# Kernel tuning notes

Measured on AMD Instinct MI355X. Metric: run time of the kernel, lower is better.

The kernel has to match this reference:

```python
import jax, jax.numpy as jnp
import numpy as np

EMB, HEADS, K, GADD, RADD = 256, 8, 8, 2, 2
REGION, STRIDE = 64, 32
MIN_SIGMA, SIGMA_SCALE, SIGMA_BOOST = 0.05, 0.1, 2.0
MMULT = 1.0 * 3.0  # clamp=True triples mmult in __init__
B, T = 4, 4096


def setup_inputs() -> dict:
    key = jax.random.key(0)
    ks = jax.random.split(key, 8)
    def lin(k, fi, fo):
        return jax.random.normal(k, (fi, fo), jnp.float32) / np.sqrt(fi).astype(np.float32)
    return {
        "x": jax.random.normal(ks[0], (B, T, EMB), jnp.float32),
        "Wq": lin(ks[1], EMB, EMB * HEADS),
        "Wk": lin(ks[2], EMB, EMB * HEADS),
        "Wv": lin(ks[3], EMB, EMB * HEADS),
        "Wu": lin(ks[4], EMB * HEADS, EMB),
        "bu": jnp.zeros((EMB,), jnp.float32),
        "W1": lin(ks[5], EMB + 1, 4 * EMB),
        "b1": jnp.zeros((4 * EMB,), jnp.float32),
        "W2": lin(ks[6], 4 * EMB, 2 * K) * 0.1,
        "b2": jnp.zeros((2 * K,), jnp.float32),
    }


def _forward(x, Wq, Wk, Wv, Wu, bu, W1, b1, W2, b2):
    b, t, e = x.shape
    h, k, r = HEADS, K, STRIDE
    tp = t // r
    vs = k * (2 + GADD + RADD)
    sel = (jnp.arange(tp) + 1) * r - 1  # query positions (tp,)

    # --- hyper network: k Gaussian means/sigmas per (strided) query position ---
    coords = jnp.broadcast_to((jnp.arange(tp, dtype=jnp.float32) / tp)[None, :, None], (b, tp, 1))
    inp = jnp.concatenate([x[:, sel, :], coords], axis=2)            # (b,tp,e+1)
    params = jax.nn.relu(inp @ W1 + b1) @ W2 + b2                    # (b,tp,2k)
    diags = sel.astype(jnp.float32)[None, :, None]                   # (1,tp,1)
    means = diags - MMULT * jax.nn.softplus(params[:, :, :k])        # (b,tp,k), left of diagonal
    means = jnp.clip(means, 0.0, t - 1.0)                            # transform_means 'clamp'
    sigmas = (jax.nn.softplus(params[:, :, k:] + SIGMA_BOOST) + MIN_SIGMA) * t * SIGMA_SCALE

    # --- ngenerate: 2 integer neighbours + global + regional samples per Gaussian ---
    kg, kr = jax.random.split(jax.random.key(42))
    fl = jnp.floor(means)                                            # (b,tp,k)
    neigh = jnp.stack([fl, fl + 1.0], axis=-1)                       # (b,tp,k,2)
    gidx = jax.random.randint(kg, (b, tp, k, GADD), 0, t).astype(jnp.float32)
    lo = jnp.clip(fl - REGION // 2, 0.0, float(t - REGION))
    ridx = lo[..., None] + jax.random.randint(kr, (b, tp, k, RADD), 0, REGION).astype(jnp.float32)
    idxf = jnp.concatenate([neigh, gidx, ridx], axis=-1)             # (b,tp,k,2+G+R)
    indices = jnp.clip(idxf, 0, t - 1).astype(jnp.int32).reshape(b, tp, vs)

    # --- densities of every sampled index under every mixture component ---
    indfl = indices.astype(jnp.float32)
    z = (indfl[:, :, :, None] - means[:, :, None, :]) / sigmas[:, :, None, :]
    props = jnp.exp(-0.5 * z * z)                                    # (b,tp,vs,k)

    # zero duplicates (keep first occurrence) and acausal indices
    eq = indices[:, :, :, None] == indices[:, :, None, :]            # (b,tp,vs,vs)
    tri = np.tril(np.ones((vs, vs), dtype=bool), -1)
    dup = jnp.any(eq & tri[None, None], axis=-1)                     # (b,tp,vs)
    valid = (~dup) & (indices <= sel[None, :, None])
    props = jnp.where(valid[..., None], props, 0.0)
    props = props / props.sum(axis=2, keepdims=True)
    weights = props.sum(axis=3)                                      # mvalues == 1 -> (b,tp,vs)

    # --- per-head projections (each head has full emb dim) ---
    scale = e ** 0.25
    qh = (x @ Wq).reshape(b, t, h, e).transpose(0, 2, 1, 3) / scale  # (b,h,t,e)
    kh = (x @ Wk).reshape(b, t, h, e).transpose(0, 2, 1, 3) / scale
    vh = (x @ Wv).reshape(b, t, h, e).transpose(0, 2, 1, 3)

    # gather sparse key/value rows
    ki = jnp.broadcast_to(indices.reshape(b, 1, tp * vs, 1), (b, h, tp * vs, e))
    skeys = jnp.take_along_axis(kh, ki, axis=2).reshape(b, h, tp, vs, e)
    svals = jnp.take_along_axis(vh, ki, axis=2).reshape(b, h, tp, vs, e)
    qsel = qh[:, :, sel, :]                                          # (b,h,tp,e)

    dot = jnp.einsum('bhpe,bhpve->bhpv', qsel, skeys)                # sparse dot products
    att = jax.nn.softmax(weights[:, None] * dot, axis=-1)            # sparse row logsoftmax().exp()
    outp = jnp.einsum('bhpv,bhpve->bhpe', att, svals)                # sparse batchmm

    out = jnp.zeros((b, h, t, e), x.dtype).at[:, :, sel, :].set(outp)
    out = out.transpose(0, 2, 1, 3).reshape(b, t, h * e)
    return out @ Wu + bu


def reference(x, Wq, Wk, Wv, Wu, bu, W1, b1, W2, b2):
    return _forward(x, Wq, Wk, Wv, Wu, bu, W1, b1, W2, b2)
```

## Files before the change

kernel.cpp:

```cpp
#include <hip/hip_runtime.h>
#include <stdint.h>

#define EMB   256
#define HEADS 8
#define KMIX  8
#define GADD  2
#define RADD  2
#define REGION 64
#define STRIDE 32
#define BB    4
#define TT    4096
#define TP    128
#define VS    48
#define HID   1024
#define NQ    2048

__device__ __forceinline__ uint32_t rotl32(uint32_t x, int d) {
  return (x << d) | (x >> (32 - d));
}
__device__ __forceinline__ void tf2x32(uint32_t k0, uint32_t k1,
                                       uint32_t x0, uint32_t x1,
                                       uint32_t& o0, uint32_t& o1) {
  uint32_t ks2 = k0 ^ k1 ^ 0x1BD11BDAu;
  x0 += k0; x1 += k1;
#define TFR(r) { x0 += x1; x1 = rotl32(x1, r); x1 ^= x0; }
  TFR(13) TFR(15) TFR(26) TFR(6)
  x0 += k1; x1 += ks2 + 1u;
  TFR(17) TFR(29) TFR(16) TFR(24)
  x0 += ks2; x1 += k0 + 2u;
  TFR(13) TFR(15) TFR(26) TFR(6)
  x0 += k0; x1 += k1 + 3u;
  TFR(17) TFR(29) TFR(16) TFR(24)
  x0 += k1; x1 += ks2 + 4u;
  TFR(13) TFR(15) TFR(26) TFR(6)
  x0 += ks2; x1 += k0 + 5u;
#undef TFR
  o0 = x0; o1 = x1;
}

__device__ __forceinline__ size_t selrow(int m) {
  return (size_t)(m >> 7) * TT + ((m & 127) * STRIDE + STRIDE - 1);
}

__global__ __launch_bounds__(256) void phase1_kernel(
    const float* __restrict__ Wq, const float* __restrict__ Wk,
    const float* __restrict__ Wv, const float* __restrict__ Wu,
    const float* __restrict__ x,  const float* __restrict__ W1,
    float* __restrict__ M8, float* __restrict__ PV, float* __restrict__ hid0)
{
  const int bid = blockIdx.x;
  const int tid = threadIdx.x;
  const int tx = tid & 15, ty = tid >> 4;

  __shared__ float As[32][33];
  __shared__ __align__(16) float Braw[64 * 33];

  float acc[2][4];
#pragma unroll
  for (int i = 0; i < 2; i++)
#pragma unroll
    for (int j = 0; j < 4; j++) acc[i][j] = 0.0f;

  if (bid < 512) {
    const int zz = bid >> 5, rem = bid & 31;
    const int n0 = (rem & 3) * 64, m0 = (rem >> 2) * 32;
    if (zz < HEADS) {
      const float* A = Wq + zz * 256;
      const float* B = Wk + zz * 256;
      float* C = M8 + (size_t)zz * EMB * EMB;
      for (int k0 = 0; k0 < EMB; k0 += 32) {
        {
          int r = tid >> 3, kq = tid & 7;
          float4 v = *(const float4*)(A + (size_t)(m0 + r) * NQ + k0 + kq * 4);
          As[r][kq * 4 + 0] = v.x; As[r][kq * 4 + 1] = v.y;
          As[r][kq * 4 + 2] = v.z; As[r][kq * 4 + 3] = v.w;
        }
#pragma unroll
        for (int rr = 0; rr < 2; rr++) {
          int c = tid * 2 + rr;
          int r = c >> 3, kq = c & 7;
          float4 v = *(const float4*)(B + (size_t)(n0 + r) * NQ + k0 + kq * 4);
          Braw[r * 33 + kq * 4 + 0] = v.x; Braw[r * 33 + kq * 4 + 1] = v.y;
          Braw[r * 33 + kq * 4 + 2] = v.z; Braw[r * 33 + kq * 4 + 3] = v.w;
        }
        __syncthreads();
#pragma unroll
        for (int kk = 0; kk < 32; kk++) {
          float a0 = As[ty * 2 + 0][kk], a1 = As[ty * 2 + 1][kk];
          float b0 = Braw[(tx * 4 + 0) * 33 + kk];
          float b1 = Braw[(tx * 4 + 1) * 33 + kk];
          float b2 = Braw[(tx * 4 + 2) * 33 + kk];
          float b3 = Braw[(tx * 4 + 3) * 33 + kk];
          acc[0][0] = fmaf(a0, b0, acc[0][0]); acc[0][1] = fmaf(a0, b1, acc[0][1]);
          acc[0][2] = fmaf(a0, b2, acc[0][2]); acc[0][3] = fmaf(a0, b3, acc[0][3]);
          acc[1][0] = fmaf(a1, b0, acc[1][0]); acc[1][1] = fmaf(a1, b1, acc[1][1]);
          acc[1][2] = fmaf(a1, b2, acc[1][2]); acc[1][3] = fmaf(a1, b3, acc[1][3]);
        }
        __syncthreads();
      }
#pragma unroll
      for (int i = 0; i < 2; i++) {
        float* cp = C + (size_t)(m0 + ty * 2 + i) * EMB + n0 + tx * 4;
        *(float4*)cp = make_float4(acc[i][0] * 0.0625f, acc[i][1] * 0.0625f,
                                   acc[i][2] * 0.0625f, acc[i][3] * 0.0625f);
      }
    } else {
      const int hh = zz - HEADS;
      const float* A = Wv + hh * 256;
      const float* W = Wu + (size_t)hh * 256 * EMB;
      float* C = PV + (size_t)hh * EMB * EMB;
      for (int k0 = 0; k0 < EMB; k0 += 32) {
        {
          int r = tid >> 3, kq = tid & 7;
          float4 v = *(const float4*)(A + (size_t)(m0 + r) * NQ + k0 + kq * 4);
          As[r][kq * 4 + 0] = v.x; As[r][kq * 4 + 1] = v.y;
          As[r][kq * 4 + 2] = v.z; As[r][kq * 4 + 3] = v.w;
        }
#pragma unroll
        for (int rr = 0; rr < 2; rr++) {
          int c = tid * 2 + rr;
          int kk = c >> 4, n4 = c & 15;
          *(float4*)(&Braw[kk * 64 + n4 * 4]) =
              *(const float4*)(W + (size_t)(k0 + kk) * EMB + n0 + n4 * 4);
        }
        __syncthreads();
#pragma unroll
        for (int kk = 0; kk < 32; kk++) {
          float a0 = As[ty * 2 + 0][kk], a1 = As[ty * 2 + 1][kk];
          float4 b4 = *(const float4*)&Braw[kk * 64 + tx * 4];
          acc[0][0] = fmaf(a0, b4.x, acc[0][0]); acc[0][1] = fmaf(a0, b4.y, acc[0][1]);
          acc[0][2] = fmaf(a0, b4.z, acc[0][2]); acc[0][3] = fmaf(a0, b4.w, acc[0][3]);
          acc[1][0] = fmaf(a1, b4.x, acc[1][0]); acc[1][1] = fmaf(a1, b4.y, acc[1][1]);
          acc[1][2] = fmaf(a1, b4.z, acc[1][2]); acc[1][3] = fmaf(a1, b4.w, acc[1][3]);
        }
        __syncthreads();
      }
#pragma unroll
      for (int i = 0; i < 2; i++) {
        float* cp = C + (size_t)(m0 + ty * 2 + i) * EMB + n0 + tx * 4;
        *(float4*)cp = make_float4(acc[i][0], acc[i][1], acc[i][2], acc[i][3]);
      }
    }
  } else {
    const int idx = bid - 512;
    const int n0 = (idx & 15) * 64, m0 = (idx >> 4) * 32;
    for (int k0 = 0; k0 < EMB; k0 += 32) {
      {
        int r = tid >> 3, kq = tid & 7;
        float4 v = *(const float4*)(x + selrow(m0 + r) * EMB + k0 + kq * 4);
        As[r][kq * 4 + 0] = v.x; As[r][kq * 4 + 1] = v.y;
        As[r][kq * 4 + 2] = v.z; As[r][kq * 4 + 3] = v.w;
      }
#pragma unroll
      for (int rr = 0; rr < 2; rr++) {
        int c = tid * 2 + rr;
        int kk = c >> 4, n4 = c & 15;
        *(float4*)(&Braw[kk * 64 + n4 * 4]) =
            *(const float4*)(W1 + (size_t)(k0 + kk) * HID + n0 + n4 * 4);
      }
      __syncthreads();
#pragma unroll
      for (int kk = 0; kk < 32; kk++) {
        float a0 = As[ty * 2 + 0][kk], a1 = As[ty * 2 + 1][kk];
        float4 b4 = *(const float4*)&Braw[kk * 64 + tx * 4];
        acc[0][0] = fmaf(a0, b4.x, acc[0][0]); acc[0][1] = fmaf(a0, b4.y, acc[0][1]);
        acc[0][2] = fmaf(a0, b4.z, acc[0][2]); acc[0][3] = fmaf(a0, b4.w, acc[0][3]);
        acc[1][0] = fmaf(a1, b4.x, acc[1][0]); acc[1][1] = fmaf(a1, b4.y, acc[1][1]);
        acc[1][2] = fmaf(a1, b4.z, acc[1][2]); acc[1][3] = fmaf(a1, b4.w, acc[1][3]);
      }
      __syncthreads();
    }
#pragma unroll
    for (int i = 0; i < 2; i++) {
      float* cp = hid0 + (size_t)(m0 + ty * 2 + i) * HID + n0 + tx * 4;
      *(float4*)cp = make_float4(acc[i][0], acc[i][1], acc[i][2], acc[i][3]);
    }
  }
}

__device__ __forceinline__ float softplus_f(float v) {
  return fmaxf(v, 0.0f) + log1pf(expf(-fabsf(v)));
}

__global__ __launch_bounds__(256) void phase2_kernel(
    const float* __restrict__ x,  const float* __restrict__ M8,
    const float* __restrict__ hid0,
    const float* __restrict__ W1, const float* __restrict__ b1,
    const float* __restrict__ W2, const float* __restrict__ b2,
    float* __restrict__ qk, int* __restrict__ idx_out, float* __restrict__ w_out)
{
  const int bid = blockIdx.x;
  const int tid = threadIdx.x;

  if (bid < 512) {
    const int h = bid >> 6, rem = bid & 63;
    const int n0 = (rem & 3) * 64, m0 = (rem >> 2) * 32;
    const int tx = tid & 15, ty = tid >> 4;
    const float* W = M8 + (size_t)h * EMB * EMB;

    __shared__ float As[32][33];
    __shared__ __align__(16) float Bs[32][64];

    float acc[2][4];
#pragma unroll
    for (int i = 0; i < 2; i++)
#pragma unroll
      for (int j = 0; j < 4; j++) acc[i][j] = 0.0f;

    for (int k0 = 0; k0 < EMB; k0 += 32) {
      {
        int r = tid >> 3, kq = tid & 7;
        float4 v = *(const float4*)(x + selrow(m0 + r) * EMB + k0 + kq * 4);
        As[r][kq * 4 + 0] = v.x; As[r][kq * 4 + 1] = v.y;
        As[r][kq * 4 + 2] = v.z; As[r][kq * 4 + 3] = v.w;
      }
#pragma unroll
      for (int rr = 0; rr < 2; rr++) {
        int c = tid * 2 + rr;
        int kk = c >> 4, n4 = c & 15;
        *(float4*)(&Bs[kk][n4 * 4]) =
            *(const float4*)(W + (size_t)(k0 + kk) * EMB + n0 + n4 * 4);
      }
      __syncthreads();
#pragma unroll
      for (int kk = 0; kk < 32; kk++) {
        float a0 = As[ty * 2 + 0][kk], a1 = As[ty * 2 + 1][kk];
        float4 b4 = *(const float4*)&Bs[kk][tx * 4];
        acc[0][0] = fmaf(a0, b4.x, acc[0][0]); acc[0][1] = fmaf(a0, b4.y, acc[0][1]);
        acc[0][2] = fmaf(a0, b4.z, acc[0][2]); acc[0][3] = fmaf(a0, b4.w, acc[0][3]);
        acc[1][0] = fmaf(a1, b4.x, acc[1][0]); acc[1][1] = fmaf(a1, b4.y, acc[1][1]);
        acc[1][2] = fmaf(a1, b4.z, acc[1][2]); acc[1][3] = fmaf(a1, b4.w, acc[1][3]);
      }
      __syncthreads();
    }
#pragma unroll
    for (int i = 0; i < 2; i++) {
      float* cp = qk + (size_t)(m0 + ty * 2 + i) * NQ + h * 256 + n0 + tx * 4;
      *(float4*)cp = make_float4(acc[i][0], acc[i][1], acc[i][2], acc[i][3]);
    }
  } else {
    const int bp = bid - 512;
    const int b = bp >> 7, p = bp & 127;
    const int selp = STRIDE * p + STRIDE - 1;
    const float coordp = (float)p / (float)TP;

    __shared__ float shid[HID];
    __shared__ float spartial[256];
    __shared__ float spar[2 * KMIX];
    __shared__ float sm[KMIX], ss[KMIX];
    __shared__ int   sidx[VS];
    __shared__ float sidxf[VS];
    __shared__ int   svalid[VS];
    __shared__ float sprops[KMIX][VS];
    __shared__ float sden[KMIX];
    __shared__ int   sgrand[16], srrand[16];

    if (tid < 16) {
      uint32_t i = (uint32_t)(bp * 16 + tid);
      uint32_t kg0, kg1, kr0, kr1, g2k0, g2k1, r2k0, r2k1, o0, o1;
      tf2x32(0u, 42u, 0u, 0u, kg0, kg1);
      tf2x32(0u, 42u, 0u, 1u, kr0, kr1);
      tf2x32(kg0, kg1, 0u, 1u, g2k0, g2k1);
      tf2x32(kr0, kr1, 0u, 1u, r2k0, r2k1);
      tf2x32(g2k0, g2k1, 0u, i, o0, o1);
      sgrand[tid] = (int)((o0 ^ o1) & 4095u);
      tf2x32(r2k0, r2k1, 0u, i, o0, o1);
      srrand[tid] = (int)((o0 ^ o1) & 63u);
    }

#pragma unroll
    for (int q = 0; q < HID / 256; q++) {
      int j = q * 256 + tid;
      shid[j] = fmaxf(hid0[(size_t)bp * HID + j] + coordp * W1[(size_t)EMB * HID + j] + b1[j], 0.0f);
    }
    __syncthreads();

    {
      int o = tid & 15, g = tid >> 4;
      float pa = 0.0f;
      for (int jj = 0; jj < 64; jj++) {
        int j = g * 64 + jj;
        pa = fmaf(shid[j], W2[j * (2 * KMIX) + o], pa);
      }
      spartial[o * 16 + g] = pa;
    }
    __syncthreads();
    if (tid < 2 * KMIX) {
      float acc = 0.0f;
      for (int g = 0; g < 16; g++) acc += spartial[tid * 16 + g];
      spar[tid] = acc + b2[tid];
    }
    __syncthreads();

    if (tid < KMIX) {
      float m = (float)selp - 3.0f * softplus_f(spar[tid]);
      m = fminf(fmaxf(m, 0.0f), (float)(TT - 1));
      sm[tid] = m;
      ss[tid] = (softplus_f(spar[KMIX + tid] + 2.0f) + 0.05f) * (float)TT * 0.1f;
    }
    __syncthreads();

    if (tid < VS) {
      int kk = tid / 6, jj = tid % 6;
      float fl = floorf(sm[kk]);
      float v;
      if (jj == 0) v = fl;
      else if (jj == 1) v = fl + 1.0f;
      else if (jj < 4) v = (float)sgrand[kk * GADD + (jj - 2)];
      else {
        float lo = fminf(fmaxf(fl - (float)(REGION / 2), 0.0f), (float)(TT - REGION));
        v = lo + (float)srrand[kk * RADD + (jj - 4)];
      }
      v = fminf(fmaxf(v, 0.0f), (float)(TT - 1));
      int ii = (int)v;
      sidx[tid] = ii;
      sidxf[tid] = (float)ii;
    }
    __syncthreads();

    if (tid < VS) {
      int d = 0;
      for (int u = 0; u < tid; u++) d |= (sidx[u] == sidx[tid]);
      svalid[tid] = (!d) && (sidx[tid] <= selp);
    }
    __syncthreads();

    for (int l = tid; l < KMIX * VS; l += 256) {
      int kk = l / VS, v = l - kk * VS;
      float zz = (sidxf[v] - sm[kk]) / ss[kk];
      sprops[kk][v] = svalid[v] ? expf(-0.5f * zz * zz) : 0.0f;
    }
    __syncthreads();
    if (tid < KMIX) {
      float den = 0.0f;
      for (int v = 0; v < VS; v++) den += sprops[tid][v];
      sden[tid] = den;
    }
    __syncthreads();

    if (tid < VS) {
      float w = 0.0f;
      for (int kk = 0; kk < KMIX; kk++) w += sprops[kk][tid] / sden[kk];
      w_out[(size_t)bp * VS + tid] = w;
      idx_out[(size_t)bp * VS + tid] = sidx[tid];
    }
  }
}

__global__ __launch_bounds__(256) void attn5_kernel(
    const float* __restrict__ x,
    const float* __restrict__ qk,
    const int* __restrict__ idx_in,
    const float* __restrict__ w_in,
    float* __restrict__ z)
{
  const int bp = blockIdx.x, b = bp >> 7;
  const int tid = threadIdx.x;
  const int wave = tid >> 6, lane = tid & 63;
  const int vsub = lane >> 4, dgrp = lane & 15;
  const int h0 = wave * 2, h1 = h0 + 1;

  __shared__ __align__(16) float xg[VS][260];
  __shared__ float part[HEADS][VS][5];
  __shared__ __align__(16) float sa[HEADS][VS];

  int myidx = 0; float myw = 0.0f;
  if (lane < VS) {
    myidx = idx_in[(size_t)bp * VS + lane];
    myw   = w_in[(size_t)bp * VS + lane];
  }

#pragma unroll
  for (int i = 0; i < 12; i++) {
    int v = wave * 12 + i;
    int row = __shfl(myidx, v, 64);
    float4 f = *(const float4*)(x + ((size_t)b * TT + row) * EMB + lane * 4);
    *(float4*)&xg[v][lane * 4] = f;
  }

  float4 q0[4], q1[4];
#pragma unroll
  for (int j = 0; j < 4; j++) {
    q0[j] = *(const float4*)(qk + (size_t)bp * NQ + h0 * 256 + dgrp * 16 + j * 4);
    q1[j] = *(const float4*)(qk + (size_t)bp * NQ + h1 * 256 + dgrp * 16 + j * 4);
  }
  __syncthreads();

#pragma unroll
  for (int it = 0; it < 12; it++) {
    int v = it * 4 + vsub;
    float p0 = 0.0f, p1 = 0.0f;
#pragma unroll
    for (int j = 0; j < 4; j++) {
      float4 xv = *(const float4*)&xg[v][dgrp * 16 + j * 4];
      p0 = fmaf(q0[j].x, xv.x, fmaf(q0[j].y, xv.y, fmaf(q0[j].z, xv.z, fmaf(q0[j].w, xv.w, p0))));
      p1 = fmaf(q1[j].x, xv.x, fmaf(q1[j].y, xv.y, fmaf(q1[j].z, xv.z, fmaf(q1[j].w, xv.w, p1))));
    }
    p0 += __shfl_xor(p0, 1, 64); p0 += __shfl_xor(p0, 2, 64);
    p1 += __shfl_xor(p1, 1, 64); p1 += __shfl_xor(p1, 2, 64);
    if ((dgrp & 3) == 0) {
      part[h0][v][dgrp >> 2] = p0;
      part[h1][v][dgrp >> 2] = p1;
    }
  }
  __syncthreads();

#pragma unroll
  for (int hh = 0; hh < 2; hh++) {
    const int h = h0 + hh;
    float logit = -1e30f;
    if (lane < VS) {
      float dot = part[h][lane][0] + part[h][lane][1] + part[h][lane][2] + part[h][lane][3];
      logit = myw * dot;
    }
    float mx = logit;
#pragma unroll
    for (int m = 32; m >= 1; m >>= 1) mx = fmaxf(mx, __shfl_xor(mx, m, 64));
    float e = (lane < VS) ? __expf(logit - mx) : 0.0f;
    float s = e;
#pragma unroll
    for (int m = 32; m >= 1; m >>= 1) s += __shfl_xor(s, m, 64);
    if (lane < VS) sa[h][lane] = e / s;
  }
  __syncthreads();

  float4 a0 = make_float4(0.f, 0.f, 0.f, 0.f);
  float4 a1 = make_float4(0.f, 0.f, 0.f, 0.f);
#pragma unroll
  for (int v0 = 0; v0 < VS; v0 += 4) {
    float4 at0 = *(const float4*)&sa[h0][v0];
    float4 at1 = *(const float4*)&sa[h1][v0];
#pragma unroll
    for (int k = 0; k < 4; k++) {
      float4 xv = *(const float4*)&xg[v0 + k][lane * 4];
      float c0 = (k == 0) ? at0.x : (k == 1) ? at0.y : (k == 2) ? at0.z : at0.w;
      float c1 = (k == 0) ? at1.x : (k == 1) ? at1.y : (k == 2) ? at1.z : at1.w;
      a0.x = fmaf(c0, xv.x, a0.x); a0.y = fmaf(c0, xv.y, a0.y);
      a0.z = fmaf(c0, xv.z, a0.z); a0.w = fmaf(c0, xv.w, a0.w);
      a1.x = fmaf(c1, xv.x, a1.x); a1.y = fmaf(c1, xv.y, a1.y);
      a1.z = fmaf(c1, xv.z, a1.z); a1.w = fmaf(c1, xv.w, a1.w);
    }
  }
  *(float4*)(z + (size_t)bp * NQ + h0 * 256 + lane * 4) = a0;
  *(float4*)(z + (size_t)bp * NQ + h1 * 256 + lane * 4) = a1;
}

__global__ __launch_bounds__(256) void gemm_nn(
    const float* __restrict__ A, int lda, size_t Az,
    const float* __restrict__ W, int ldw, size_t Wz,
    float* __restrict__ C, int ldc, size_t Cz,
    int kLen)
{
  A += (size_t)blockIdx.z * Az;
  W += (size_t)blockIdx.z * Wz;
  C += (size_t)blockIdx.z * Cz;
  const int tid = threadIdx.x;
  const int tx = tid & 15, ty = tid >> 4;
  const int n0 = blockIdx.x * 64, m0 = blockIdx.y * 32;

  __shared__ float As[32][33];
  __shared__ __align__(16) float Bs[32][64];

  float acc[2][4];
#pragma unroll
  for (int i = 0; i < 2; i++)
#pragma unroll
    for (int j = 0; j < 4; j++) acc[i][j] = 0.0f;

  for (int k0 = 0; k0 < kLen; k0 += 32) {
    {
      int r = tid >> 3, kq = tid & 7;
      float4 v = *(const float4*)(A + (size_t)(m0 + r) * lda + k0 + kq * 4);
      As[r][kq * 4 + 0] = v.x; As[r][kq * 4 + 1] = v.y;
      As[r][kq * 4 + 2] = v.z; As[r][kq * 4 + 3] = v.w;
    }
#pragma unroll
    for (int rr = 0; rr < 2; rr++) {
      int c = tid * 2 + rr;
      int kk = c >> 4, n4 = c & 15;
      *(float4*)(&Bs[kk][n4 * 4]) =
          *(const float4*)(W + (size_t)(k0 + kk) * ldw + n0 + n4 * 4);
    }
    __syncthreads();
#pragma unroll
    for (int kk = 0; kk < 32; kk++) {
      float a0 = As[ty * 2 + 0][kk];
      float a1 = As[ty * 2 + 1][kk];
      float4 b4 = *(const float4*)&Bs[kk][tx * 4];
      acc[0][0] = fmaf(a0, b4.x, acc[0][0]);
      acc[0][1] = fmaf(a0, b4.y, acc[0][1]);
      acc[0][2] = fmaf(a0, b4.z, acc[0][2]);
      acc[0][3] = fmaf(a0, b4.w, acc[0][3]);
      acc[1][0] = fmaf(a1, b4.x, acc[1][0]);
      acc[1][1] = fmaf(a1, b4.y, acc[1][1]);
      acc[1][2] = fmaf(a1, b4.z, acc[1][2]);
      acc[1][3] = fmaf(a1, b4.w, acc[1][3]);
    }
    __syncthreads();
  }

#pragma unroll
  for (int i = 0; i < 2; i++) {
    float* cp = C + (size_t)(m0 + ty * 2 + i) * ldc + n0 + tx * 4;
    *(float4*)cp = make_float4(acc[i][0], acc[i][1], acc[i][2], acc[i][3]);
  }
}

__global__ __launch_bounds__(256) void final_out(
    const float* __restrict__ part,
    const float* __restrict__ bu,
    float* __restrict__ out)
{
  int i4 = blockIdx.x * 256 + threadIdx.x;
  const int e4 = i4 & 63;
  const int row = i4 >> 6;
  const int t = row & (TT - 1), b = row >> 12;
  float4 r = ((const float4*)bu)[e4];
  if ((t & 31) == 31) {
    const int bp = b * TP + (t >> 5);
#pragma unroll
    for (int h = 0; h < HEADS; h++) {
      float4 pv = *(const float4*)&part[((size_t)h * (BB * TP) + bp) * EMB + e4 * 4];
      r.x += pv.x; r.y += pv.y; r.z += pv.z; r.w += pv.w;
    }
  }
  ((float4*)out)[i4] = r;
}

extern "C" void kernel_launch(void* const* d_in, const int* in_sizes, int n_in,
                              void* d_out, int out_size, void* d_ws, size_t ws_size,
                              hipStream_t stream) {
  const float* x  = (const float*)d_in[0];
  const float* Wq = (const float*)d_in[1];
  const float* Wk = (const float*)d_in[2];
  const float* Wv = (const float*)d_in[3];
  const float* Wu = (const float*)d_in[4];
  const float* bu = (const float*)d_in[5];
  const float* W1 = (const float*)d_in[6];
  const float* b1 = (const float*)d_in[7];
  const float* W2 = (const float*)d_in[8];
  const float* b2 = (const float*)d_in[9];
  float* out = (float*)d_out;

  char* ws = (char*)d_ws;
  size_t off = 0;
  auto alloc = [&](size_t bytes) { char* p = ws + off; off += (bytes + 255) & ~(size_t)255; return p; };
  float* hid0  = (float*)alloc((size_t)BB * TP * HID * 4);
  float* M8    = (float*)alloc((size_t)HEADS * EMB * EMB * 4);
  float* PV    = (float*)alloc((size_t)HEADS * EMB * EMB * 4);
  float* qk    = (float*)alloc((size_t)BB * TP * NQ * 4);
  float* zbuf  = (float*)alloc((size_t)BB * TP * NQ * 4);
  float* part  = (float*)alloc((size_t)HEADS * BB * TP * EMB * 4);
  int*   idxb  = (int*)  alloc((size_t)BB * TP * VS * 4);
  float* wts   = (float*)alloc((size_t)BB * TP * VS * 4);

  phase1_kernel<<<dim3(768), dim3(256), 0, stream>>>(
      Wq, Wk, Wv, Wu, x, W1, M8, PV, hid0);

  phase2_kernel<<<dim3(1024), dim3(256), 0, stream>>>(
      x, M8, hid0, W1, b1, W2, b2, qk, idxb, wts);

  attn5_kernel<<<dim3(BB * TP), dim3(256), 0, stream>>>(
      x, qk, idxb, wts, zbuf);

  gemm_nn<<<dim3(EMB / 64, (BB * TP) / 32, HEADS), dim3(256), 0, stream>>>(
      zbuf, NQ, 256, PV, EMB, (size_t)EMB * EMB, part, EMB, (size_t)BB * TP * EMB, EMB);

  final_out<<<dim3((BB * TT * EMB / 4) / 256), dim3(256), 0, stream>>>(
      part, bu, out);
}
```

Before: 74.67 us.

## Fold bias fill into first kernel and accumulate head projections atomically

The output bias broadcast now runs as extra blocks appended to the first kernel's grid, so the output is initialised early. The per-head output-projection GEMM scatters its results with float atomicAdd straight into the selected output rows. This removes the partial-sum buffer and the separate final reduction kernel, cutting one launch and a round trip through the partial buffer. In exchange there are 8-way atomic contention per output element and a summation order that is no longer deterministic.

```diff
diff --git a/kernel.cpp b/kernel.cpp
--- a/kernel.cpp
+++ b/kernel.cpp
@@ -42,16 +42,24 @@
   return (size_t)(m >> 7) * TT + ((m & 127) * STRIDE + STRIDE - 1);
 }
 
-__global__ __launch_bounds__(256) void phase1_kernel(
+__global__ __launch_bounds__(256) void mega1_kernel(
     const float* __restrict__ Wq, const float* __restrict__ Wk,
     const float* __restrict__ Wv, const float* __restrict__ Wu,
     const float* __restrict__ x,  const float* __restrict__ W1,
-    float* __restrict__ M8, float* __restrict__ PV, float* __restrict__ hid0)
+    const float* __restrict__ bu,
+    float* __restrict__ M8, float* __restrict__ PV, float* __restrict__ hid0,
+    float* __restrict__ out)
 {
   const int bid = blockIdx.x;
   const int tid = threadIdx.x;
+
+  if (bid >= 768) {
+    int i4 = (bid - 768) * 256 + tid;
+    ((float4*)out)[i4] = ((const float4*)bu)[i4 & 63];
+    return;
+  }
+
   const int tx = tid & 15, ty = tid >> 4;
-
   __shared__ float As[32][33];
   __shared__ __align__(16) float Braw[64 * 33];
 
@@ -445,15 +453,14 @@
   *(float4*)(z + (size_t)bp * NQ + h1 * 256 + lane * 4) = a1;
 }
 
-__global__ __launch_bounds__(256) void gemm_nn(
-    const float* __restrict__ A, int lda, size_t Az,
-    const float* __restrict__ W, int ldw, size_t Wz,
-    float* __restrict__ C, int ldc, size_t Cz,
-    int kLen)
+__global__ __launch_bounds__(256) void pv_atomic(
+    const float* __restrict__ z,
+    const float* __restrict__ PV,
+    float* __restrict__ out)
 {
-  A += (size_t)blockIdx.z * Az;
-  W += (size_t)blockIdx.z * Wz;
-  C += (size_t)blockIdx.z * Cz;
+  const int h = blockIdx.z;
+  const float* A = z + h * 256;
+  const float* W = PV + (size_t)h * EMB * EMB;
   const int tid = threadIdx.x;
   const int tx = tid & 15, ty = tid >> 4;
   const int n0 = blockIdx.x * 64, m0 = blockIdx.y * 32;
@@ -467,10 +474,10 @@
 #pragma unroll
     for (int j = 0; j < 4; j++) acc[i][j] = 0.0f;
 
-  for (int k0 = 0; k0 < kLen; k0 += 32) {
+  for (int k0 = 0; k0 < EMB; k0 += 32) {
     {
       int r = tid >> 3, kq = tid & 7;
-      float4 v = *(const float4*)(A + (size_t)(m0 + r) * lda + k0 + kq * 4);
+      float4 v = *(const float4*)(A + (size_t)(m0 + r) * NQ + k0 + kq * 4);
       As[r][kq * 4 + 0] = v.x; As[r][kq * 4 + 1] = v.y;
       As[r][kq * 4 + 2] = v.z; As[r][kq * 4 + 3] = v.w;
     }
@@ -479,7 +486,7 @@
       int c = tid * 2 + rr;
       int kk = c >> 4, n4 = c & 15;
       *(float4*)(&Bs[kk][n4 * 4]) =
-          *(const float4*)(W + (size_t)(k0 + kk) * ldw + n0 + n4 * 4);
+          *(const float4*)(W + (size_t)(k0 + kk) * EMB + n0 + n4 * 4);
     }
     __syncthreads();
 #pragma unroll
@@ -501,30 +508,11 @@
 
 #pragma unroll
   for (int i = 0; i < 2; i++) {
-    float* cp = C + (size_t)(m0 + ty * 2 + i) * ldc + n0 + tx * 4;
-    *(float4*)cp = make_float4(acc[i][0], acc[i][1], acc[i][2], acc[i][3]);
-  }
-}
-
-__global__ __launch_bounds__(256) void final_out(
-    const float* __restrict__ part,
-    const float* __restrict__ bu,
-    float* __restrict__ out)
-{
-  int i4 = blockIdx.x * 256 + threadIdx.x;
-  const int e4 = i4 & 63;
-  const int row = i4 >> 6;
-  const int t = row & (TT - 1), b = row >> 12;
-  float4 r = ((const float4*)bu)[e4];
-  if ((t & 31) == 31) {
-    const int bp = b * TP + (t >> 5);
-#pragma unroll
-    for (int h = 0; h < HEADS; h++) {
-      float4 pv = *(const float4*)&part[((size_t)h * (BB * TP) + bp) * EMB + e4 * 4];
-      r.x += pv.x; r.y += pv.y; r.z += pv.z; r.w += pv.w;
-    }
-  }
-  ((float4*)out)[i4] = r;
+    float* cp = out + selrow(m0 + ty * 2 + i) * EMB + n0 + tx * 4;
+#pragma unroll
+    for (int j = 0; j < 4; j++)
+      atomicAdd(cp + j, acc[i][j]);
+  }
 }
 
 extern "C" void kernel_launch(void* const* d_in, const int* in_sizes, int n_in,
@@ -550,12 +538,11 @@
   float* PV    = (float*)alloc((size_t)HEADS * EMB * EMB * 4);
   float* qk    = (float*)alloc((size_t)BB * TP * NQ * 4);
   float* zbuf  = (float*)alloc((size_t)BB * TP * NQ * 4);
-  float* part  = (float*)alloc((size_t)HEADS * BB * TP * EMB * 4);
   int*   idxb  = (int*)  alloc((size_t)BB * TP * VS * 4);
   float* wts   = (float*)alloc((size_t)BB * TP * VS * 4);
 
-  phase1_kernel<<<dim3(768), dim3(256), 0, stream>>>(
-      Wq, Wk, Wv, Wu, x, W1, M8, PV, hid0);
+  mega1_kernel<<<dim3(768 + (BB * TT * EMB / 4) / 256), dim3(256), 0, stream>>>(
+      Wq, Wk, Wv, Wu, x, W1, bu, M8, PV, hid0, out);
 
   phase2_kernel<<<dim3(1024), dim3(256), 0, stream>>>(
       x, M8, hid0, W1, b1, W2, b2, qk, idxb, wts);
@@ -563,9 +550,6 @@
   attn5_kernel<<<dim3(BB * TP), dim3(256), 0, stream>>>(
       x, qk, idxb, wts, zbuf);
 
-  gemm_nn<<<dim3(EMB / 64, (BB * TP) / 32, HEADS), dim3(256), 0, stream>>>(
-      zbuf, NQ, 256, PV, EMB, (size_t)EMB * EMB, part, EMB, (size_t)BB * TP * EMB, EMB);
-
-  final_out<<<dim3((BB * TT * EMB / 4) / 256), dim3(256), 0, stream>>>(
-      part, bu, out);
-}
+  pv_atomic<<<dim3(EMB / 64, (BB * TP) / 32, HEADS), dim3(256), 0, stream>>>(
+      zbuf, PV, out);
+}
```

Measured after the change: 80.19 us. 7.4% more time.
